# Optimization experiments

Hardware: AMD Instinct MI355X
Metric: run time of the kernel (lower is better)

## Reference

```python
import jax, jax.numpy as jnp
import numpy as np

INPUT_DIM = 1024
EMBED_DIM = 1024
NUM_HEADS = 16
HEAD_DIM = EMBED_DIM // NUM_HEADS


def _xavier_uniform(key, shape):
    fan_in, fan_out = shape[1], shape[0]
    limit = float(np.sqrt(6.0 / (fan_in + fan_out)))
    return jax.random.uniform(key, shape, jnp.float32, -limit, limit)


def setup_inputs() -> dict:
    key = jax.random.key(0)
    kx, kqkv, ko = jax.random.split(key, 3)
    x = jax.random.normal(kx, (2, 2048, INPUT_DIM), jnp.float32)
    # torch Linear stores weight as [out, in]; we keep that convention
    w_qkv = _xavier_uniform(kqkv, (3 * EMBED_DIM, INPUT_DIM))
    b_qkv = jnp.zeros((3 * EMBED_DIM,), jnp.float32)
    w_o = _xavier_uniform(ko, (EMBED_DIM, EMBED_DIM))
    b_o = jnp.zeros((EMBED_DIM,), jnp.float32)
    return {"x": x, "w_qkv": w_qkv, "b_qkv": b_qkv, "w_o": w_o, "b_o": b_o}


def reference(x, w_qkv, b_qkv, w_o, b_o):
    B, S, _ = x.shape
    H, D = NUM_HEADS, HEAD_DIM
    qkv = jnp.einsum("bsi,oi->bso", x, w_qkv) + b_qkv          # [B,S,3E]
    qkv = qkv.reshape(B, S, H, 3 * D).transpose(0, 2, 1, 3)    # [B,H,S,3D]
    q, k, v = jnp.split(qkv, 3, axis=-1)                        # each [B,H,S,D]
    scores = jnp.einsum("bhqd,bhkd->bhqk", q, k) / jnp.sqrt(jnp.float32(D))
    attn = jax.nn.softmax(scores, axis=-1)                      # [B,H,S,S]
    vals = jnp.einsum("bhqk,bhkd->bhqd", attn, v)               # [B,H,S,D]
    vals = vals.transpose(0, 2, 1, 3).reshape(B, S, H * D)      # [B,S,E]
    return jnp.einsum("bse,oe->bso", vals, w_o) + b_o
```

## Files before the change

kernel.cpp:

```cpp
#include <hip/hip_runtime.h>
#include <hip/hip_bf16.h>


typedef __attribute__((ext_vector_type(8))) short bf16x8;
typedef __attribute__((ext_vector_type(4))) short bf16x4;
typedef __attribute__((ext_vector_type(4))) float f32x4;

#define MFMA16(a, b, c) __builtin_amdgcn_mfma_f32_16x16x32_bf16((a), (b), (c), 0, 0, 0)

#if __has_builtin(__builtin_amdgcn_exp2f)
#define EXP2F(x) __builtin_amdgcn_exp2f(x)
#else
#define EXP2F(x) exp2f(x)
#endif

static __device__ __forceinline__ unsigned short f2bf_bits(float v) {
    __hip_bfloat16 h = __float2bfloat16(v);
    return *reinterpret_cast<unsigned short*>(&h);
}

static __device__ __forceinline__ bf16x8 cvt8(const float* p) {
    const f32x4 a = reinterpret_cast<const f32x4*>(p)[0];
    const f32x4 b = reinterpret_cast<const f32x4*>(p)[1];
    bf16x8 r;
    r[0] = (short)f2bf_bits(a[0]); r[1] = (short)f2bf_bits(a[1]);
    r[2] = (short)f2bf_bits(a[2]); r[3] = (short)f2bf_bits(a[3]);
    r[4] = (short)f2bf_bits(b[0]); r[5] = (short)f2bf_bits(b[1]);
    r[6] = (short)f2bf_bits(b[2]); r[7] = (short)f2bf_bits(b[3]);
    return r;
}

__device__ __forceinline__ bf16x8 ldg8(const __hip_bfloat16* p) {
    return *reinterpret_cast<const bf16x8*>(p);
}

__global__ __launch_bounds__(256)
void cast_f32_bf16(const float* __restrict__ src, __hip_bfloat16* __restrict__ dst) {
    const size_t base = ((size_t)blockIdx.x * 256 + threadIdx.x) * 32;
#pragma unroll
    for (int i = 0; i < 4; ++i)
        *reinterpret_cast<bf16x8*>(dst + base + i * 8) = cvt8(src + base + i * 8);
}

__global__ __launch_bounds__(256)
void qkv_gemm(const __hip_bfloat16* __restrict__ xb,
              const __hip_bfloat16* __restrict__ wb,
              const float* __restrict__ bqkv,
              __hip_bfloat16* __restrict__ Q,
              __hip_bfloat16* __restrict__ K,
              __hip_bfloat16* __restrict__ Vt) {
    __shared__ unsigned short As[128 * 40];
    __shared__ unsigned short Bs[128 * 40];

    const int tid  = threadIdx.x;
    const int lane = tid & 63;
    const int wv   = tid >> 6;
    const int quad = lane >> 4;
    const int l16  = lane & 15;
    const int wm   = wv >> 1;
    const int wn   = wv & 1;

    const int bid = blockIdx.x;
    const int xcd = bid & 7;
    const int r   = bid >> 3;
    const int m0  = (r / 3) * 128;
    const int n0  = (xcd * 3 + (r % 3)) * 128;

    const int sr = tid >> 1;
    const int sc = (tid & 1) * 16;
    const __hip_bfloat16* ag = xb + (size_t)(m0 + sr) * 1024 + sc;
    const __hip_bfloat16* bg = wb + (size_t)(n0 + sr) * 1024 + sc;
    unsigned short* aw = &As[sr * 40 + sc];
    unsigned short* bw = &Bs[sr * 40 + sc];

    f32x4 zv = {0.f, 0.f, 0.f, 0.f};
    f32x4 acc[4][4];
#pragma unroll
    for (int ii = 0; ii < 4; ++ii)
#pragma unroll
        for (int jj = 0; jj < 4; ++jj) acc[ii][jj] = zv;

    for (int k0 = 0; k0 < 1024; k0 += 32) {
        const bf16x8 av0 = ldg8(ag + k0), av1 = ldg8(ag + k0 + 8);
        const bf16x8 bv0 = ldg8(bg + k0), bv1 = ldg8(bg + k0 + 8);
        __syncthreads();
        reinterpret_cast<bf16x8*>(aw)[0] = av0;
        reinterpret_cast<bf16x8*>(aw)[1] = av1;
        reinterpret_cast<bf16x8*>(bw)[0] = bv0;
        reinterpret_cast<bf16x8*>(bw)[1] = bv1;
        __syncthreads();
        bf16x8 af[4], bf[4];
#pragma unroll
        for (int ii = 0; ii < 4; ++ii)
            af[ii] = *reinterpret_cast<const bf16x8*>(
                &As[(wm * 64 + ii * 16 + l16) * 40 + quad * 8]);
#pragma unroll
        for (int jj = 0; jj < 4; ++jj)
            bf[jj] = *reinterpret_cast<const bf16x8*>(
                &Bs[(wn * 64 + jj * 16 + l16) * 40 + quad * 8]);
#pragma unroll
        for (int ii = 0; ii < 4; ++ii)
#pragma unroll
            for (int jj = 0; jj < 4; ++jj)
                acc[ii][jj] = MFMA16(af[ii], bf[jj], acc[ii][jj]);
    }

    const float QSCALE = 0.18033688011f;

#pragma unroll
    for (int jj = 0; jj < 4; ++jj) {
        const int n = n0 + wn * 64 + jj * 16 + l16;
        const float bias = bqkv[n];
        const int h = n / 192;
        const int r2 = n - h * 192;
        const int t = r2 >> 6;
        const int d = r2 & 63;
#pragma unroll
        for (int ii = 0; ii < 4; ++ii) {
#pragma unroll
            for (int i = 0; i < 4; ++i) {
                const int m = m0 + wm * 64 + ii * 16 + quad * 4 + i;
                const int b = m >> 11;
                const int s = m & 2047;
                const int bh = b * 16 + h;
                float v = acc[ii][jj][i] + bias;
                if (t == 0) {
                    Q[((size_t)bh * 2048 + s) * 64 + d] = __float2bfloat16(v * QSCALE);
                } else if (t == 1) {
                    K[((size_t)bh * 2048 + s) * 64 + d] = __float2bfloat16(v);
                } else {
                    Vt[((size_t)bh * 64 + d) * 2048 + s] = __float2bfloat16(v);
                }
            }
        }
    }
}

__global__ __launch_bounds__(256)
void attn_kernel(const __hip_bfloat16* __restrict__ Q,
                 const __hip_bfloat16* __restrict__ K,
                 const __hip_bfloat16* __restrict__ Vt,
                 __hip_bfloat16* __restrict__ AO) {
    __shared__ unsigned short Ks0[32 * 40];
    __shared__ unsigned short Ks1[32 * 40];
    __shared__ unsigned short Vs[64 * 40];

    const int tid  = threadIdx.x;
    const int lane = tid & 63;
    const int wv   = tid >> 6;
    const int quad = lane >> 4;
    const int l16  = lane & 15;

    const int blk = blockIdx.x;
    const int xcd = blk & 7;
    const int sub = blk >> 3;
    const int bh  = xcd * 4 + (sub & 3);
    const int qb  = sub >> 2;
    const int q0  = qb * 128 + wv * 32;
    const int b   = bh >> 4;
    const int h   = bh & 15;

    const __hip_bfloat16* Qp = Q  + (size_t)bh * 131072;
    const __hip_bfloat16* Kp = K  + (size_t)bh * 131072;
    const __hip_bfloat16* Vp = Vt + (size_t)bh * 131072;

    bf16x8 bQ[2][2];
#pragma unroll
    for (int t = 0; t < 2; ++t)
#pragma unroll
        for (int dh = 0; dh < 2; ++dh)
            bQ[t][dh] = ldg8(Qp + (size_t)(q0 + t * 16 + l16) * 64 + dh * 32 + quad * 8);

    const int kr = tid >> 3;
    const int kc = (tid & 7) * 8;
    const int kb = kr & 7;
    const int sig = (kb < 4) ? ((kr >> 3) * 4 + kb) : (16 + (kr >> 3) * 4 + (kb - 4));
    unsigned short* kw = (kc < 32) ? &Ks0[sig * 40 + kc] : &Ks1[sig * 40 + (kc - 32)];
    const int vr = tid >> 2;
    const int vc = (tid & 3) * 8;
    unsigned short* vw = &Vs[vr * 40 + vc];

    f32x4 zv = {0.f, 0.f, 0.f, 0.f};
    f32x4 Of[2][4];
#pragma unroll
    for (int t = 0; t < 2; ++t)
#pragma unroll
        for (int jj = 0; jj < 4; ++jj) Of[t][jj] = zv;
    float li[2] = {0.f, 0.f};

    for (int kt = 0; kt < 64; ++kt) {
        const int key0 = kt * 32;

        const bf16x8 gk = ldg8(Kp + (size_t)(key0 + kr) * 64 + kc);
        const bf16x8 gv = ldg8(Vp + (size_t)vr * 2048 + key0 + vc);
        __syncthreads();
        *reinterpret_cast<bf16x8*>(kw) = gk;
        *reinterpret_cast<bf16x8*>(vw) = gv;
        __syncthreads();

        const bf16x8 aKA0 = *reinterpret_cast<const bf16x8*>(&Ks0[l16 * 40 + quad * 8]);
        const bf16x8 aKA1 = *reinterpret_cast<const bf16x8*>(&Ks1[l16 * 40 + quad * 8]);
        const bf16x8 aKB0 = *reinterpret_cast<const bf16x8*>(&Ks0[(16 + l16) * 40 + quad * 8]);
        const bf16x8 aKB1 = *reinterpret_cast<const bf16x8*>(&Ks1[(16 + l16) * 40 + quad * 8]);
        bf16x8 aV[4];
#pragma unroll
        for (int jj = 0; jj < 4; ++jj)
            aV[jj] = *reinterpret_cast<const bf16x8*>(&Vs[(jj * 16 + l16) * 40 + quad * 8]);

        f32x4 sA[2], sB[2];
#pragma unroll
        for (int t = 0; t < 2; ++t) {
            sA[t] = zv; sB[t] = zv;
            sA[t] = MFMA16(aKA0, bQ[t][0], sA[t]);
            sA[t] = MFMA16(aKA1, bQ[t][1], sA[t]);
            sB[t] = MFMA16(aKB0, bQ[t][0], sB[t]);
            sB[t] = MFMA16(aKB1, bQ[t][1], sB[t]);
        }

#pragma unroll
        for (int t = 0; t < 2; ++t) {
            float pA[4], pB[4];
#pragma unroll
            for (int i = 0; i < 4; ++i) {
                pA[i] = EXP2F(sA[t][i]);
                pB[i] = EXP2F(sB[t][i]);
            }
            li[t] += ((pA[0] + pA[1]) + (pA[2] + pA[3]))
                   + ((pB[0] + pB[1]) + (pB[2] + pB[3]));

            bf16x8 bP;
            bP[0] = (short)f2bf_bits(pA[0]); bP[1] = (short)f2bf_bits(pA[1]);
            bP[2] = (short)f2bf_bits(pA[2]); bP[3] = (short)f2bf_bits(pA[3]);
            bP[4] = (short)f2bf_bits(pB[0]); bP[5] = (short)f2bf_bits(pB[1]);
            bP[6] = (short)f2bf_bits(pB[2]); bP[7] = (short)f2bf_bits(pB[3]);

#pragma unroll
            for (int jj = 0; jj < 4; ++jj)
                Of[t][jj] = MFMA16(aV[jj], bP, Of[t][jj]);
        }
    }

#pragma unroll
    for (int t = 0; t < 2; ++t) {
        li[t] += __shfl_xor(li[t], 16);
        li[t] += __shfl_xor(li[t], 32);
    }

#pragma unroll
    for (int t = 0; t < 2; ++t) {
        const float linv = 1.f / li[t];
        const int s = q0 + t * 16 + l16;
        __hip_bfloat16* aop = AO + (((size_t)b * 2048 + s) * 16 + h) * 64;
#pragma unroll
        for (int jj = 0; jj < 4; ++jj) {
            bf16x4 pk;
#pragma unroll
            for (int i = 0; i < 4; ++i)
                pk[i] = (short)f2bf_bits(Of[t][jj][i] * linv);
            *reinterpret_cast<bf16x4*>(aop + jj * 16 + quad * 4) = pk;
        }
    }
}

__global__ __launch_bounds__(256)
void out_gemm(const __hip_bfloat16* __restrict__ A,
              const __hip_bfloat16* __restrict__ wob,
              const float* __restrict__ bo,
              float* __restrict__ out) {
    __shared__ unsigned short As[128 * 40];
    __shared__ unsigned short Bs[128 * 40];

    const int tid  = threadIdx.x;
    const int lane = tid & 63;
    const int wv   = tid >> 6;
    const int quad = lane >> 4;
    const int l16  = lane & 15;
    const int wm   = wv >> 1;
    const int wn   = wv & 1;

    const int bid = blockIdx.x;
    const int m0  = (bid >> 3) * 128;
    const int n0  = (bid & 7) * 128;

    const int sr = tid >> 1;
    const int sc = (tid & 1) * 16;
    const __hip_bfloat16* ag = A   + (size_t)(m0 + sr) * 1024 + sc;
    const __hip_bfloat16* bg = wob + (size_t)(n0 + sr) * 1024 + sc;
    unsigned short* aw = &As[sr * 40 + sc];
    unsigned short* bw = &Bs[sr * 40 + sc];

    f32x4 zv = {0.f, 0.f, 0.f, 0.f};
    f32x4 acc[4][4];
#pragma unroll
    for (int ii = 0; ii < 4; ++ii)
#pragma unroll
        for (int jj = 0; jj < 4; ++jj) acc[ii][jj] = zv;

    for (int k0 = 0; k0 < 1024; k0 += 32) {
        const bf16x8 av0 = ldg8(ag + k0), av1 = ldg8(ag + k0 + 8);
        const bf16x8 bv0 = ldg8(bg + k0), bv1 = ldg8(bg + k0 + 8);
        __syncthreads();
        reinterpret_cast<bf16x8*>(aw)[0] = av0;
        reinterpret_cast<bf16x8*>(aw)[1] = av1;
        reinterpret_cast<bf16x8*>(bw)[0] = bv0;
        reinterpret_cast<bf16x8*>(bw)[1] = bv1;
        __syncthreads();
        bf16x8 af[4], bf[4];
#pragma unroll
        for (int ii = 0; ii < 4; ++ii)
            af[ii] = *reinterpret_cast<const bf16x8*>(
                &As[(wm * 64 + ii * 16 + l16) * 40 + quad * 8]);
#pragma unroll
        for (int jj = 0; jj < 4; ++jj)
            bf[jj] = *reinterpret_cast<const bf16x8*>(
                &Bs[(wn * 64 + jj * 16 + l16) * 40 + quad * 8]);
#pragma unroll
        for (int ii = 0; ii < 4; ++ii)
#pragma unroll
            for (int jj = 0; jj < 4; ++jj)
                acc[ii][jj] = MFMA16(af[ii], bf[jj], acc[ii][jj]);
    }

#pragma unroll
    for (int jj = 0; jj < 4; ++jj) {
        const int n = n0 + wn * 64 + jj * 16 + l16;
        const float bias = bo[n];
#pragma unroll
        for (int ii = 0; ii < 4; ++ii) {
#pragma unroll
            for (int i = 0; i < 4; ++i) {
                const int m = m0 + wm * 64 + ii * 16 + quad * 4 + i;
                out[(size_t)m * 1024 + n] = acc[ii][jj][i] + bias;
            }
        }
    }
}

extern "C" void kernel_launch(void* const* d_in, const int* in_sizes, int n_in,
                              void* d_out, int out_size, void* d_ws, size_t ws_size,
                              hipStream_t stream) {
    const float* x    = (const float*)d_in[0];
    const float* wqkv = (const float*)d_in[1];
    const float* bqkv = (const float*)d_in[2];
    const float* wo   = (const float*)d_in[3];
    const float* bo   = (const float*)d_in[4];
    float* out = (float*)d_out;

    __hip_bfloat16* ws = (__hip_bfloat16*)d_ws;
    __hip_bfloat16* Q   = ws;
    __hip_bfloat16* K   = ws + (size_t)4194304;
    __hip_bfloat16* Vt  = ws + (size_t)8388608;
    __hip_bfloat16* AO  = ws + (size_t)12582912;
    __hip_bfloat16* wob = Q;

    __hip_bfloat16* xb     = (__hip_bfloat16*)d_out;
    __hip_bfloat16* wqkvb  = xb + (size_t)4194304;

    cast_f32_bf16<<<dim3(512), 256, 0, stream>>>(x, xb);
    cast_f32_bf16<<<dim3(384), 256, 0, stream>>>(wqkv, wqkvb);
    qkv_gemm<<<dim3(768), 256, 0, stream>>>(xb, wqkvb, bqkv, Q, K, Vt);
    attn_kernel<<<dim3(512), 256, 0, stream>>>(Q, K, Vt, AO);
    cast_f32_bf16<<<dim3(128), 256, 0, stream>>>(wo, wob);
    out_gemm<<<dim3(256), 256, 0, stream>>>(AO, wob, bo, out);
}
```

Before: 218.1 us.

## Use direct global-to-LDS loads in GEMMs, halve out_gemm tile, merge cast launches

Both GEMMs now stage A/B tiles through global_load_lds instead of loading into registers and then storing to shared memory. The LDS padding is dropped to a 32-element stride to match the direct-load layout, which may reintroduce bank conflicts on the fragment reads. out_gemm uses 64-row M tiles and twice as many blocks for better CU occupancy. The two input cast kernels are fused into one launch to cut launch overhead.

```diff
diff --git a/kernel.cpp b/kernel.cpp
--- a/kernel.cpp
+++ b/kernel.cpp
@@ -34,6 +34,25 @@
     return *reinterpret_cast<const bf16x8*>(p);
 }
 
+__device__ __forceinline__ void load16_lds(const __hip_bfloat16* g, unsigned short* l) {
+    __builtin_amdgcn_global_load_lds(
+        (const __attribute__((address_space(1))) void*)g,
+        (__attribute__((address_space(3))) void*)l, 16, 0, 0);
+}
+
+__global__ __launch_bounds__(256)
+void cast2_f32_bf16(const float* __restrict__ x, __hip_bfloat16* __restrict__ xb,
+                    const float* __restrict__ w, __hip_bfloat16* __restrict__ wb) {
+    const int bid = blockIdx.x;
+    const float* src = (bid < 512) ? x : w;
+    __hip_bfloat16* dst = (bid < 512) ? xb : wb;
+    const int rb = (bid < 512) ? bid : (bid - 512);
+    const size_t base = (size_t)rb * 8192 + (size_t)threadIdx.x * 32;
+#pragma unroll
+    for (int i = 0; i < 4; ++i)
+        *reinterpret_cast<bf16x8*>(dst + base + i * 8) = cvt8(src + base + i * 8);
+}
+
 __global__ __launch_bounds__(256)
 void cast_f32_bf16(const float* __restrict__ src, __hip_bfloat16* __restrict__ dst) {
     const size_t base = ((size_t)blockIdx.x * 256 + threadIdx.x) * 32;
@@ -49,8 +68,8 @@
               __hip_bfloat16* __restrict__ Q,
               __hip_bfloat16* __restrict__ K,
               __hip_bfloat16* __restrict__ Vt) {
-    __shared__ unsigned short As[128 * 40];
-    __shared__ unsigned short Bs[128 * 40];
+    __shared__ unsigned short As[128 * 32];
+    __shared__ unsigned short Bs[128 * 32];
 
     const int tid  = threadIdx.x;
     const int lane = tid & 63;
@@ -66,12 +85,12 @@
     const int m0  = (r / 3) * 128;
     const int n0  = (xcd * 3 + (r % 3)) * 128;
 
-    const int sr = tid >> 1;
-    const int sc = (tid & 1) * 16;
-    const __hip_bfloat16* ag = xb + (size_t)(m0 + sr) * 1024 + sc;
-    const __hip_bfloat16* bg = wb + (size_t)(n0 + sr) * 1024 + sc;
-    unsigned short* aw = &As[sr * 40 + sc];
-    unsigned short* bw = &Bs[sr * 40 + sc];
+    const __hip_bfloat16* agl = xb + (size_t)(m0 + wv * 32 + (lane >> 2)) * 1024 + (lane & 3) * 8;
+    const __hip_bfloat16* bgl = wb + (size_t)(n0 + wv * 32 + (lane >> 2)) * 1024 + (lane & 3) * 8;
+    unsigned short* al0 = &As[(wv * 32) * 32];
+    unsigned short* al1 = &As[(wv * 32 + 16) * 32];
+    unsigned short* bl0 = &Bs[(wv * 32) * 32];
+    unsigned short* bl1 = &Bs[(wv * 32 + 16) * 32];
 
     f32x4 zv = {0.f, 0.f, 0.f, 0.f};
     f32x4 acc[4][4];
@@ -81,28 +100,26 @@
         for (int jj = 0; jj < 4; ++jj) acc[ii][jj] = zv;
 
     for (int k0 = 0; k0 < 1024; k0 += 32) {
-        const bf16x8 av0 = ldg8(ag + k0), av1 = ldg8(ag + k0 + 8);
-        const bf16x8 bv0 = ldg8(bg + k0), bv1 = ldg8(bg + k0 + 8);
-        __syncthreads();
-        reinterpret_cast<bf16x8*>(aw)[0] = av0;
-        reinterpret_cast<bf16x8*>(aw)[1] = av1;
-        reinterpret_cast<bf16x8*>(bw)[0] = bv0;
-        reinterpret_cast<bf16x8*>(bw)[1] = bv1;
+        load16_lds(agl + k0, al0);
+        load16_lds(agl + 16 * 1024 + k0, al1);
+        load16_lds(bgl + k0, bl0);
+        load16_lds(bgl + 16 * 1024 + k0, bl1);
         __syncthreads();
         bf16x8 af[4], bf[4];
 #pragma unroll
         for (int ii = 0; ii < 4; ++ii)
             af[ii] = *reinterpret_cast<const bf16x8*>(
-                &As[(wm * 64 + ii * 16 + l16) * 40 + quad * 8]);
+                &As[(wm * 64 + ii * 16 + l16) * 32 + quad * 8]);
 #pragma unroll
         for (int jj = 0; jj < 4; ++jj)
             bf[jj] = *reinterpret_cast<const bf16x8*>(
-                &Bs[(wn * 64 + jj * 16 + l16) * 40 + quad * 8]);
+                &Bs[(wn * 64 + jj * 16 + l16) * 32 + quad * 8]);
 #pragma unroll
         for (int ii = 0; ii < 4; ++ii)
 #pragma unroll
             for (int jj = 0; jj < 4; ++jj)
                 acc[ii][jj] = MFMA16(af[ii], bf[jj], acc[ii][jj]);
+        __syncthreads();
     }
 
     const float QSCALE = 0.18033688011f;
@@ -267,8 +284,8 @@
               const __hip_bfloat16* __restrict__ wob,
               const float* __restrict__ bo,
               float* __restrict__ out) {
-    __shared__ unsigned short As[128 * 40];
-    __shared__ unsigned short Bs[128 * 40];
+    __shared__ unsigned short As[64 * 32];
+    __shared__ unsigned short Bs[128 * 32];
 
     const int tid  = threadIdx.x;
     const int lane = tid & 63;
@@ -279,46 +296,42 @@
     const int wn   = wv & 1;
 
     const int bid = blockIdx.x;
-    const int m0  = (bid >> 3) * 128;
+    const int m0  = (bid >> 3) * 64;
     const int n0  = (bid & 7) * 128;
 
-    const int sr = tid >> 1;
-    const int sc = (tid & 1) * 16;
-    const __hip_bfloat16* ag = A   + (size_t)(m0 + sr) * 1024 + sc;
-    const __hip_bfloat16* bg = wob + (size_t)(n0 + sr) * 1024 + sc;
-    unsigned short* aw = &As[sr * 40 + sc];
-    unsigned short* bw = &Bs[sr * 40 + sc];
+    const __hip_bfloat16* agl = A   + (size_t)(m0 + wv * 16 + (lane >> 2)) * 1024 + (lane & 3) * 8;
+    const __hip_bfloat16* bgl = wob + (size_t)(n0 + wv * 32 + (lane >> 2)) * 1024 + (lane & 3) * 8;
+    unsigned short* al0 = &As[(wv * 16) * 32];
+    unsigned short* bl0 = &Bs[(wv * 32) * 32];
+    unsigned short* bl1 = &Bs[(wv * 32 + 16) * 32];
 
     f32x4 zv = {0.f, 0.f, 0.f, 0.f};
-    f32x4 acc[4][4];
-#pragma unroll
-    for (int ii = 0; ii < 4; ++ii)
+    f32x4 acc[2][4];
+#pragma unroll
+    for (int ii = 0; ii < 2; ++ii)
 #pragma unroll
         for (int jj = 0; jj < 4; ++jj) acc[ii][jj] = zv;
 
     for (int k0 = 0; k0 < 1024; k0 += 32) {
-        const bf16x8 av0 = ldg8(ag + k0), av1 = ldg8(ag + k0 + 8);
-        const bf16x8 bv0 = ldg8(bg + k0), bv1 = ldg8(bg + k0 + 8);
-        __syncthreads();
-        reinterpret_cast<bf16x8*>(aw)[0] = av0;
-        reinterpret_cast<bf16x8*>(aw)[1] = av1;
-        reinterpret_cast<bf16x8*>(bw)[0] = bv0;
-        reinterpret_cast<bf16x8*>(bw)[1] = bv1;
-        __syncthreads();
-        bf16x8 af[4], bf[4];
-#pragma unroll
-        for (int ii = 0; ii < 4; ++ii)
+        load16_lds(agl + k0, al0);
+        load16_lds(bgl + k0, bl0);
+        load16_lds(bgl + 16 * 1024 + k0, bl1);
+        __syncthreads();
+        bf16x8 af[2], bf[4];
+#pragma unroll
+        for (int ii = 0; ii < 2; ++ii)
             af[ii] = *reinterpret_cast<const bf16x8*>(
-                &As[(wm * 64 + ii * 16 + l16) * 40 + quad * 8]);
+                &As[(wm * 32 + ii * 16 + l16) * 32 + quad * 8]);
 #pragma unroll
         for (int jj = 0; jj < 4; ++jj)
             bf[jj] = *reinterpret_cast<const bf16x8*>(
-                &Bs[(wn * 64 + jj * 16 + l16) * 40 + quad * 8]);
-#pragma unroll
-        for (int ii = 0; ii < 4; ++ii)
+                &Bs[(wn * 64 + jj * 16 + l16) * 32 + quad * 8]);
+#pragma unroll
+        for (int ii = 0; ii < 2; ++ii)
 #pragma unroll
             for (int jj = 0; jj < 4; ++jj)
                 acc[ii][jj] = MFMA16(af[ii], bf[jj], acc[ii][jj]);
+        __syncthreads();
     }
 
 #pragma unroll
@@ -326,10 +339,10 @@
         const int n = n0 + wn * 64 + jj * 16 + l16;
         const float bias = bo[n];
 #pragma unroll
-        for (int ii = 0; ii < 4; ++ii) {
+        for (int ii = 0; ii < 2; ++ii) {
 #pragma unroll
             for (int i = 0; i < 4; ++i) {
-                const int m = m0 + wm * 64 + ii * 16 + quad * 4 + i;
+                const int m = m0 + wm * 32 + ii * 16 + quad * 4 + i;
                 out[(size_t)m * 1024 + n] = acc[ii][jj][i] + bias;
             }
         }
@@ -356,10 +369,9 @@
     __hip_bfloat16* xb     = (__hip_bfloat16*)d_out;
     __hip_bfloat16* wqkvb  = xb + (size_t)4194304;
 
-    cast_f32_bf16<<<dim3(512), 256, 0, stream>>>(x, xb);
-    cast_f32_bf16<<<dim3(384), 256, 0, stream>>>(wqkv, wqkvb);
+    cast2_f32_bf16<<<dim3(896), 256, 0, stream>>>(x, xb, wqkv, wqkvb);
     qkv_gemm<<<dim3(768), 256, 0, stream>>>(xb, wqkvb, bqkv, Q, K, Vt);
     attn_kernel<<<dim3(512), 256, 0, stream>>>(Q, K, Vt, AO);
     cast_f32_bf16<<<dim3(128), 256, 0, stream>>>(wo, wob);
-    out_gemm<<<dim3(256), 256, 0, stream>>>(AO, wob, bo, out);
-}
+    out_gemm<<<dim3(512), 256, 0, stream>>>(AO, wob, bo, out);
+}
```

Measured after the change: 203.2 us. 6.8% less time.
